# Optimization experiments

Hardware: AMD Instinct MI355X
Metric: run time of the kernel (lower is better)

## Reference

```python
import jax, jax.numpy as jnp
import numpy as np

N = 100000   # nodes
E = 1600000  # edges (avg degree 16)
D = 128      # in_feats == h_feats (residual requires equality)
RES = 0.2    # residual coefficient
EPS = 1e-5   # LayerNorm eps (torch default)
PROP_STEP = 3


def setup_inputs() -> dict:
    key = jax.random.key(0)
    ks = jax.random.split(key, 8)
    s = 1.0 / np.sqrt(D)
    return {
        "src": jax.random.randint(ks[0], (E,), 0, N),
        "dst": jax.random.randint(ks[1], (E,), 0, N),
        "in_feat": jax.random.normal(ks[2], (N, D), jnp.float32),
        # conv1 / conv2 GraphConv weights (Glorot-ish scale) and biases
        "W1": jax.random.normal(ks[3], (D, D), jnp.float32) * s,
        "b1": jnp.zeros((D,), jnp.float32),
        "W2": jax.random.normal(ks[4], (D, D), jnp.float32) * s,
        "b2": jnp.zeros((D,), jnp.float32),
        # LayerNorms used at loop steps i=1 and i=2 (norms[0] is unused by forward)
        "ln1_g": jnp.ones((D,), jnp.float32),
        "ln1_b": jnp.zeros((D,), jnp.float32),
        "ln2_g": jnp.ones((D,), jnp.float32),
        "ln2_b": jnp.zeros((D,), jnp.float32),
    }


def _gcn_conv(src, dst, x, W, b):
    # DGL GraphConv with norm='both': out = D_in^{-1/2} A D_out^{-1/2} X W + b
    ones_e = jnp.ones(src.shape[0], x.dtype)
    deg_out = jnp.maximum(jax.ops.segment_sum(ones_e, src, num_segments=N), 1.0)
    deg_in = jnp.maximum(jax.ops.segment_sum(ones_e, dst, num_segments=N), 1.0)
    xw = (x * jax.lax.rsqrt(deg_out)[:, None]) @ W           # [N, D]
    agg = jax.ops.segment_sum(xw[src], dst, num_segments=N)  # gather -> scatter-add
    return agg * jax.lax.rsqrt(deg_in)[:, None] + b


def _layer_norm(x, g, b):
    mu = jnp.mean(x, axis=-1, keepdims=True)
    var = jnp.mean(jnp.square(x - mu), axis=-1, keepdims=True)
    return (x - mu) * jax.lax.rsqrt(var + EPS) * g + b


def reference(src, dst, in_feat, W1, b1, W2, b2, ln1_g, ln1_b, ln2_g, ln2_b):
    h = _gcn_conv(src, dst, in_feat, W1, b1) + RES * in_feat
    for g_, b_ in ((ln1_g, ln1_b), (ln2_g, ln2_b)):  # steps i = 1 .. prop_step-1
        h = _layer_norm(h, g_, b_)
        h = jax.nn.relu(h)
        h = _gcn_conv(src, dst, h, W2, b2) + RES * in_feat
    return h
```

## Files before the change

kernel.cpp:

```cpp
#include <hip/hip_runtime.h>

#define NN 100000
#define DD 128
#define RESC 0.2f
#define EPSL 1e-5f
#define BSH 10
#define NBKT ((NN + 1023) >> BSH)

typedef _Float16 f16;
typedef _Float16 f16x2 __attribute__((ext_vector_type(2)));
typedef _Float16 f16x4 __attribute__((ext_vector_type(4)));
typedef _Float16 f16x8 __attribute__((ext_vector_type(8)));
typedef float f32x16 __attribute__((ext_vector_type(16)));

static __device__ __forceinline__ int swz(int r, int c_half) {
  return r * 256 + ((c_half * 2) ^ ((r & 15) << 4));
}

__global__ __launch_bounds__(256) void k_hist(const int* __restrict__ src,
                                              const int* __restrict__ dst,
                                              int* __restrict__ dego,
                                              int* __restrict__ bsum, int E) {
  __shared__ int cnt[NBKT];
  const int t = threadIdx.x;
  if (t < NBKT) cnt[t] = 0;
  __syncthreads();
  const int base = blockIdx.x * 4096 + t * 16;
#pragma unroll
  for (int q = 0; q < 4; ++q) {
    int idx = base + q * 4;
    int sv[4], dv[4];
    if (idx + 3 < E) {
      *(int4*)sv = *(const int4*)(src + idx);
      *(int4*)dv = *(const int4*)(dst + idx);
#pragma unroll
      for (int k = 0; k < 4; ++k) {
        atomicAdd(&dego[sv[k]], 1);
        atomicAdd(&cnt[dv[k] >> BSH], 1);
      }
    } else {
      for (int k = 0; k < 4 && idx + k < E; ++k) {
        atomicAdd(&dego[src[idx + k]], 1);
        atomicAdd(&cnt[dst[idx + k] >> BSH], 1);
      }
    }
  }
  __syncthreads();
  if (t < NBKT && cnt[t]) atomicAdd(&bsum[t], cnt[t]);
}

__global__ __launch_bounds__(128) void k_scan2(const int* __restrict__ bsum,
                                               int* __restrict__ bpre,
                                               int* __restrict__ bcur) {
  __shared__ int sh[128];
  const int t = threadIdx.x;
  int v = (t < NBKT) ? bsum[t] : 0;
  sh[t] = v;
  __syncthreads();
  for (int off = 1; off < 128; off <<= 1) {
    int add = (t >= off) ? sh[t - off] : 0;
    __syncthreads();
    sh[t] += add;
    __syncthreads();
  }
  if (t < NBKT) {
    int e = (t == 0) ? 0 : sh[t - 1];
    bpre[t] = e;
    bcur[t] = e;
  }
}

__global__ __launch_bounds__(256) void k_prep(const int* __restrict__ dego,
                                              float* __restrict__ rsq_o) {
  int i = blockIdx.x * 256 + threadIdx.x;
  if (i < NN) rsq_o[i] = rsqrtf((float)max(dego[i], 1));
}

__global__ __launch_bounds__(256) void k_wprep(const float* __restrict__ W,
                                               f16* __restrict__ Wt) {
  int i = blockIdx.x * 256 + threadIdx.x;
  int n = i >> 7, k = i & 127;
  Wt[(size_t)n * 128 + k] = (f16)W[(size_t)k * 128 + n];
}

__global__ __launch_bounds__(256) void k_binA(const int* __restrict__ src,
                                              const int* __restrict__ dst,
                                              int* __restrict__ bcur,
                                              int2* __restrict__ gpairs, int E) {
  __shared__ int cnt[NBKT], cnt2[NBKT], gofs[NBKT];
  const int t = threadIdx.x;
  if (t < NBKT) { cnt[t] = 0; cnt2[t] = 0; }
  __syncthreads();
  const int base = blockIdx.x * 4096 + t * 16;
  int sv[16], dv[16];
#pragma unroll
  for (int q = 0; q < 4; ++q) {
    int idx = base + q * 4;
    if (idx + 3 < E) {
      *(int4*)(sv + q * 4) = *(const int4*)(src + idx);
      *(int4*)(dv + q * 4) = *(const int4*)(dst + idx);
    } else {
#pragma unroll
      for (int k = 0; k < 4; ++k) {
        sv[q * 4 + k] = (idx + k < E) ? src[idx + k] : 0;
        dv[q * 4 + k] = (idx + k < E) ? dst[idx + k] : -1;
      }
    }
  }
#pragma unroll
  for (int j = 0; j < 16; ++j)
    if (base + j < E) atomicAdd(&cnt[dv[j] >> BSH], 1);
  __syncthreads();
  if (t < NBKT && cnt[t]) gofs[t] = atomicAdd(&bcur[t], cnt[t]);
  __syncthreads();
#pragma unroll
  for (int j = 0; j < 16; ++j)
    if (base + j < E) {
      int b = dv[j] >> BSH;
      int p = gofs[b] + atomicAdd(&cnt2[b], 1);
      gpairs[p] = make_int2(sv[j], dv[j]);
    }
}

__global__ __launch_bounds__(256) void k_binB(const int2* __restrict__ gpairs,
                                              const int* __restrict__ bpre,
                                              const int* __restrict__ bsum,
                                              int* __restrict__ rowp,
                                              float* __restrict__ rsq_i,
                                              int* __restrict__ colx, int E) {
  __shared__ int hist[1024];
  __shared__ int part[256];
  const int b = blockIdx.x, t = threadIdx.x;
  const int node0 = b << BSH;
  const int ebase = bpre[b], ecnt = bsum[b];
  for (int j = t; j < 1024; j += 256) hist[j] = 0;
  __syncthreads();
  for (int i = t; i < ecnt; i += 256)
    atomicAdd(&hist[gpairs[ebase + i].y - node0], 1);
  __syncthreads();
  const int j0 = t * 4;
  const int h0 = hist[j0], h1 = hist[j0 + 1], h2 = hist[j0 + 2], h3 = hist[j0 + 3];
  part[t] = h0 + h1 + h2 + h3;
  __syncthreads();
  for (int off = 1; off < 256; off <<= 1) {
    int add = (t >= off) ? part[t - off] : 0;
    __syncthreads();
    part[t] += add;
    __syncthreads();
  }
  int run = ebase + ((t == 0) ? 0 : part[t - 1]);
  const int pos[4] = {run, run + h0, run + h0 + h1, run + h0 + h1 + h2};
  const int hh[4] = {h0, h1, h2, h3};
#pragma unroll
  for (int k = 0; k < 4; ++k) {
    int node = node0 + j0 + k;
    if (node < NN) {
      rowp[node] = pos[k];
      rsq_i[node] = rsqrtf((float)max(hh[k], 1));
    }
  }
#pragma unroll
  for (int k = 0; k < 4; ++k) hist[j0 + k] = pos[k];
  __syncthreads();
  for (int i = t; i < ecnt; i += 256) {
    int2 pr = gpairs[ebase + i];
    int p = atomicAdd(&hist[pr.y - node0], 1);
    colx[p] = pr.x;
  }
  if (b == NBKT - 1 && t == 0) rowp[NN] = ebase + ecnt;
}

template <bool SCALE>
__global__ __launch_bounds__(256, 2) void k_gemm16(const void* __restrict__ inp,
                                                   const f16* __restrict__ Wt,
                                                   const float* __restrict__ rsq_o,
                                                   f16* __restrict__ out) {
  extern __shared__ char smem[];
  char* sX = smem;
  char* sW = smem + 32768;
  const int tid = threadIdx.x;
  const int row0 = blockIdx.x * 128;

#pragma unroll
  for (int i = 0; i < 8; ++i) {
    int chunk = i * 256 + tid;
    int r = chunk >> 4, cc = (chunk & 15) * 8;
    f16x8 v = *(const f16x8*)(Wt + (size_t)r * 128 + cc);
    *(f16x8*)(sW + swz(r, cc)) = v;
  }
#pragma unroll
  for (int i = 0; i < 8; ++i) {
    int chunk = i * 256 + tid;
    int r = chunk >> 4, cc = (chunk & 15) * 8;
    int grow = row0 + r;
    f16x8 v;
    if (SCALE) {
      const float* in = (const float*)inp;
      float4 v0 = {0, 0, 0, 0}, v1 = {0, 0, 0, 0};
      float s = 0.f;
      if (grow < NN) {
        v0 = *(const float4*)(in + (size_t)grow * DD + cc);
        v1 = *(const float4*)(in + (size_t)grow * DD + cc + 4);
        s = rsq_o[grow];
      }
      v[0] = (f16)(v0.x * s); v[1] = (f16)(v0.y * s);
      v[2] = (f16)(v0.z * s); v[3] = (f16)(v0.w * s);
      v[4] = (f16)(v1.x * s); v[5] = (f16)(v1.y * s);
      v[6] = (f16)(v1.z * s); v[7] = (f16)(v1.w * s);
    } else {
      const f16* in = (const f16*)inp;
      if (grow < NN) v = *(const f16x8*)(in + (size_t)grow * DD + cc);
      else { f16x8 z = {}; v = z; }
    }
    *(f16x8*)(sX + swz(r, cc)) = v;
  }
  __syncthreads();

  const int wv = tid >> 6, lane = tid & 63;
  const int am = lane & 31;
  const int kg = lane >> 5;
  f32x16 acc[4];
#pragma unroll
  for (int ct = 0; ct < 4; ++ct)
#pragma unroll
    for (int q = 0; q < 16; ++q) acc[ct][q] = 0.f;

  const int ar = wv * 32 + am;
#pragma unroll
  for (int ks = 0; ks < 8; ++ks) {
    const int kc = ks * 16 + kg * 8;
    f16x8 af = *(const f16x8*)(sX + swz(ar, kc));
#pragma unroll
    for (int ct = 0; ct < 4; ++ct) {
      f16x8 bf = *(const f16x8*)(sW + swz(ct * 32 + am, kc));
      acc[ct] = __builtin_amdgcn_mfma_f32_32x32x16_f16(af, bf, acc[ct], 0, 0, 0);
    }
  }

#pragma unroll
  for (int ct = 0; ct < 4; ++ct) {
#pragma unroll
    for (int reg = 0; reg < 16; ++reg) {
      int trow = (reg & 3) + 8 * (reg >> 2) + 4 * kg;
      int grow = row0 + wv * 32 + trow;
      if (grow < NN) out[(size_t)grow * DD + ct * 32 + am] = (f16)acc[ct][reg];
    }
  }
}

template <bool PRE>
__global__ __launch_bounds__(256) void k_gather(const f16* __restrict__ xw,
                                                const int* __restrict__ colx,
                                                const int* __restrict__ rowp,
                                                const float* __restrict__ rsq_i,
                                                const float* __restrict__ bias,
                                                const float* __restrict__ resid,
                                                const float* __restrict__ rsq_o,
                                                const float* __restrict__ g,
                                                const float* __restrict__ bb,
                                                void* __restrict__ outp) {
  const int wave = (blockIdx.x * 256 + threadIdx.x) >> 6;
  const int lane = threadIdx.x & 63;
  const int half = lane >> 5;
  const int l32 = lane & 31;
  if (wave >= NN) return;
  const int beg = rowp[wave], end = rowp[wave + 1];
  float4 a0 = {0, 0, 0, 0}, a1 = {0, 0, 0, 0}, a2 = {0, 0, 0, 0}, a3 = {0, 0, 0, 0};
  int e = beg + half;
  for (; e + 6 < end; e += 8) {
    int c0 = colx[e], c1 = colx[e + 2], c2 = colx[e + 4], c3 = colx[e + 6];
    f16x4 v0 = *(const f16x4*)(xw + (size_t)c0 * DD + l32 * 4);
    f16x4 v1 = *(const f16x4*)(xw + (size_t)c1 * DD + l32 * 4);
    f16x4 v2 = *(const f16x4*)(xw + (size_t)c2 * DD + l32 * 4);
    f16x4 v3 = *(const f16x4*)(xw + (size_t)c3 * DD + l32 * 4);
    a0.x += (float)v0[0]; a0.y += (float)v0[1]; a0.z += (float)v0[2]; a0.w += (float)v0[3];
    a1.x += (float)v1[0]; a1.y += (float)v1[1]; a1.z += (float)v1[2]; a1.w += (float)v1[3];
    a2.x += (float)v2[0]; a2.y += (float)v2[1]; a2.z += (float)v2[2]; a2.w += (float)v2[3];
    a3.x += (float)v3[0]; a3.y += (float)v3[1]; a3.z += (float)v3[2]; a3.w += (float)v3[3];
  }
  for (; e < end; e += 2) {
    int c = colx[e];
    f16x4 v = *(const f16x4*)(xw + (size_t)c * DD + l32 * 4);
    a0.x += (float)v[0]; a0.y += (float)v[1]; a0.z += (float)v[2]; a0.w += (float)v[3];
  }
  a0.x += a1.x + a2.x + a3.x;
  a0.y += a1.y + a2.y + a3.y;
  a0.z += a1.z + a2.z + a3.z;
  a0.w += a1.w + a2.w + a3.w;
  a0.x += __shfl_xor(a0.x, 32);
  a0.y += __shfl_xor(a0.y, 32);
  a0.z += __shfl_xor(a0.z, 32);
  a0.w += __shfl_xor(a0.w, 32);

  const float r = rsq_i[wave];
  float4 bv = *(const float4*)(bias + l32 * 4);
  float4 rf = *(const float4*)(resid + (size_t)wave * DD + l32 * 4);
  float4 o;
  o.x = a0.x * r + bv.x + RESC * rf.x;
  o.y = a0.y * r + bv.y + RESC * rf.y;
  o.z = a0.z * r + bv.z + RESC * rf.z;
  o.w = a0.w * r + bv.w + RESC * rf.w;

  if (PRE) {
    float s = o.x + o.y + o.z + o.w;
    float q = o.x * o.x + o.y * o.y + o.z * o.z + o.w * o.w;
#pragma unroll
    for (int off = 1; off < 32; off <<= 1) {
      s += __shfl_xor(s, off);
      q += __shfl_xor(q, off);
    }
    float mu = s * (1.f / 128.f);
    float var = q * (1.f / 128.f) - mu * mu;
    float rs = rsqrtf(var + EPSL);
    float sc = rsq_o[wave];
    float4 gv = *(const float4*)(g + l32 * 4);
    float4 lv = *(const float4*)(bb + l32 * 4);
    o.x = fmaxf((o.x - mu) * rs * gv.x + lv.x, 0.f) * sc;
    o.y = fmaxf((o.y - mu) * rs * gv.y + lv.y, 0.f) * sc;
    o.z = fmaxf((o.z - mu) * rs * gv.z + lv.z, 0.f) * sc;
    o.w = fmaxf((o.w - mu) * rs * gv.w + lv.w, 0.f) * sc;
    if (half == 0) {
      f16x4 o4;
      o4[0] = (f16)o.x; o4[1] = (f16)o.y; o4[2] = (f16)o.z; o4[3] = (f16)o.w;
      *(f16x4*)((f16*)outp + (size_t)wave * DD + l32 * 4) = o4;
    }
  } else {
    if (half == 0) *(float4*)((float*)outp + (size_t)wave * DD + l32 * 4) = o;
  }
}

extern "C" void kernel_launch(void* const* d_in, const int* in_sizes, int n_in,
                              void* d_out, int out_size, void* d_ws, size_t ws_size,
                              hipStream_t stream) {
  const int* src = (const int*)d_in[0];
  const int* dst = (const int*)d_in[1];
  const float* in_feat = (const float*)d_in[2];
  const float* W1 = (const float*)d_in[3];
  const float* b1 = (const float*)d_in[4];
  const float* W2 = (const float*)d_in[5];
  const float* b2 = (const float*)d_in[6];
  const float* g1 = (const float*)d_in[7];
  const float* lb1 = (const float*)d_in[8];
  const float* g2 = (const float*)d_in[9];
  const float* lb2 = (const float*)d_in[10];
  const int E = in_sizes[0];

  char* p = (char*)d_ws;
  auto alloc = [&](size_t bytes) {
    char* q = p;
    p += (bytes + 255) & ~(size_t)255;
    return q;
  };
  f16*   xw    = (f16*)alloc((size_t)NN * DD * 2);
  f16*   hb    = (f16*)alloc((size_t)NN * DD * 2);
  float* rsq_o = (float*)alloc((size_t)NN * 4);
  float* rsq_i = (float*)alloc((size_t)NN * 4);
  int*   dego  = (int*)alloc((size_t)NN * 4);
  int*   rowp  = (int*)alloc((size_t)(NN + 1) * 4);
  int*   colx  = (int*)alloc((size_t)E * 4);
  int*   bsum  = (int*)alloc((size_t)NBKT * 4);
  int*   bpre  = (int*)alloc((size_t)NBKT * 4);
  int*   bcur  = (int*)alloc((size_t)NBKT * 4);
  f16*   Wt1   = (f16*)alloc((size_t)DD * DD * 2);
  f16*   Wt2   = (f16*)alloc((size_t)DD * DD * 2);
  if ((size_t)(p - (char*)d_ws) > ws_size) return;
  int2* gpairs = (int2*)xw;

  hipMemsetAsync(dego, 0, (size_t)NN * 4, stream);
  hipMemsetAsync(bsum, 0, (size_t)NBKT * 4, stream);

  const int eb = (E + 4095) / 4096;
  k_hist<<<eb, 256, 0, stream>>>(src, dst, dego, bsum, E);
  k_scan2<<<1, 128, 0, stream>>>(bsum, bpre, bcur);
  k_prep<<<(NN + 255) / 256, 256, 0, stream>>>(dego, rsq_o);
  k_wprep<<<64, 256, 0, stream>>>(W1, Wt1);
  k_wprep<<<64, 256, 0, stream>>>(W2, Wt2);
  k_binA<<<eb, 256, 0, stream>>>(src, dst, bcur, gpairs, E);
  k_binB<<<NBKT, 256, 0, stream>>>(gpairs, bpre, bsum, rowp, rsq_i, colx, E);

  const int gblk = (NN + 127) / 128;
  const int agblk = (NN * 64 + 255) / 256;
  const size_t ldsb = 65536;

  k_gemm16<true><<<gblk, 256, ldsb, stream>>>(in_feat, Wt1, rsq_o, xw);
  k_gather<true><<<agblk, 256, 0, stream>>>(xw, colx, rowp, rsq_i, b1, in_feat, rsq_o, g1, lb1, hb);
  k_gemm16<false><<<gblk, 256, ldsb, stream>>>(hb, Wt2, rsq_o, xw);
  k_gather<true><<<agblk, 256, 0, stream>>>(xw, colx, rowp, rsq_i, b2, in_feat, rsq_o, g2, lb2, hb);
  k_gemm16<false><<<gblk, 256, ldsb, stream>>>(hb, Wt2, rsq_o, xw);
  k_gather<false><<<agblk, 256, 0, stream>>>(xw, colx, rowp, rsq_i, b2, in_feat, rsq_o, nullptr, nullptr, d_out);
}
```

Before: 520.8 us.

## Fuse gather+LayerNorm into GEMM and replace bucket scan with fixed slabs

The preprocessing drops the separate histogram, scan and prep kernels. Each destination bucket now gets a fixed slab of SLAB edges, so offsets no longer need a prefix sum, and out-degree counting is folded into the binning pass. The per-layer gather, LayerNorm and ReLU are fused with the following GEMM: each block aggregates its 128 rows into shared memory and then runs MFMA, which removes the intermediate hb round trip and a launch. The cost is a fixed per-bucket capacity that silently drops edges if a bucket overflows, and a gather phase with only 8 waves per CU of parallelism inside the GEMM kernel.

Measured after the change: 756.1 us. 45.2% more time.

```diff
diff --git a/kernel.cpp b/kernel.cpp
--- a/kernel.cpp
+++ b/kernel.cpp
@@ -6,87 +6,32 @@
 #define EPSL 1e-5f
 #define BSH 10
 #define NBKT ((NN + 1023) >> BSH)
+#define SLAB 20480
 
 typedef _Float16 f16;
-typedef _Float16 f16x2 __attribute__((ext_vector_type(2)));
 typedef _Float16 f16x4 __attribute__((ext_vector_type(4)));
 typedef _Float16 f16x8 __attribute__((ext_vector_type(8)));
 typedef float f32x16 __attribute__((ext_vector_type(16)));
 
-static __device__ __forceinline__ int swz(int r, int c_half) {
-  return r * 256 + ((c_half * 2) ^ ((r & 15) << 4));
-}
-
-__global__ __launch_bounds__(256) void k_hist(const int* __restrict__ src,
-                                              const int* __restrict__ dst,
-                                              int* __restrict__ dego,
-                                              int* __restrict__ bsum, int E) {
-  __shared__ int cnt[NBKT];
-  const int t = threadIdx.x;
-  if (t < NBKT) cnt[t] = 0;
-  __syncthreads();
-  const int base = blockIdx.x * 4096 + t * 16;
-#pragma unroll
-  for (int q = 0; q < 4; ++q) {
-    int idx = base + q * 4;
-    int sv[4], dv[4];
-    if (idx + 3 < E) {
-      *(int4*)sv = *(const int4*)(src + idx);
-      *(int4*)dv = *(const int4*)(dst + idx);
-#pragma unroll
-      for (int k = 0; k < 4; ++k) {
-        atomicAdd(&dego[sv[k]], 1);
-        atomicAdd(&cnt[dv[k] >> BSH], 1);
-      }
-    } else {
-      for (int k = 0; k < 4 && idx + k < E; ++k) {
-        atomicAdd(&dego[src[idx + k]], 1);
-        atomicAdd(&cnt[dst[idx + k] >> BSH], 1);
-      }
-    }
-  }
-  __syncthreads();
-  if (t < NBKT && cnt[t]) atomicAdd(&bsum[t], cnt[t]);
-}
-
-__global__ __launch_bounds__(128) void k_scan2(const int* __restrict__ bsum,
-                                               int* __restrict__ bpre,
+static __device__ __forceinline__ int swzb(int r, int b) {
+  return r * 256 + (b ^ ((r & 15) << 4));
+}
+
+__global__ __launch_bounds__(256) void k_wprep(const float* __restrict__ W1, const float* __restrict__ W2,
+                                               f16* __restrict__ Wt1, f16* __restrict__ Wt2,
                                                int* __restrict__ bcur) {
-  __shared__ int sh[128];
-  const int t = threadIdx.x;
-  int v = (t < NBKT) ? bsum[t] : 0;
-  sh[t] = v;
-  __syncthreads();
-  for (int off = 1; off < 128; off <<= 1) {
-    int add = (t >= off) ? sh[t - off] : 0;
-    __syncthreads();
-    sh[t] += add;
-    __syncthreads();
-  }
-  if (t < NBKT) {
-    int e = (t == 0) ? 0 : sh[t - 1];
-    bpre[t] = e;
-    bcur[t] = e;
-  }
-}
-
-__global__ __launch_bounds__(256) void k_prep(const int* __restrict__ dego,
-                                              float* __restrict__ rsq_o) {
   int i = blockIdx.x * 256 + threadIdx.x;
-  if (i < NN) rsq_o[i] = rsqrtf((float)max(dego[i], 1));
-}
-
-__global__ __launch_bounds__(256) void k_wprep(const float* __restrict__ W,
-                                               f16* __restrict__ Wt) {
-  int i = blockIdx.x * 256 + threadIdx.x;
-  int n = i >> 7, k = i & 127;
-  Wt[(size_t)n * 128 + k] = (f16)W[(size_t)k * 128 + n];
-}
-
-__global__ __launch_bounds__(256) void k_binA(const int* __restrict__ src,
-                                              const int* __restrict__ dst,
-                                              int* __restrict__ bcur,
-                                              int2* __restrict__ gpairs, int E) {
+  if (i < NBKT) bcur[i] = i * SLAB;
+  int w = i >> 14, j = i & 16383;
+  int n = j >> 7, k = j & 127;
+  const float* W = w ? W2 : W1;
+  f16* Wt = w ? Wt2 : Wt1;
+  Wt[n * 128 + k] = (f16)W[k * 128 + n];
+}
+
+__global__ __launch_bounds__(256) void k_histA(const int* __restrict__ src, const int* __restrict__ dst,
+                                               int* __restrict__ dego, int* __restrict__ bcur,
+                                               int2* __restrict__ gpairs, int E) {
   __shared__ int cnt[NBKT], cnt2[NBKT], gofs[NBKT];
   const int t = threadIdx.x;
   if (t < NBKT) { cnt[t] = 0; cnt2[t] = 0; }
@@ -109,7 +54,10 @@
   }
 #pragma unroll
   for (int j = 0; j < 16; ++j)
-    if (base + j < E) atomicAdd(&cnt[dv[j] >> BSH], 1);
+    if (base + j < E) {
+      atomicAdd(&dego[sv[j]], 1);
+      atomicAdd(&cnt[dv[j] >> BSH], 1);
+    }
   __syncthreads();
   if (t < NBKT && cnt[t]) gofs[t] = atomicAdd(&bcur[t], cnt[t]);
   __syncthreads();
@@ -118,21 +66,21 @@
     if (base + j < E) {
       int b = dv[j] >> BSH;
       int p = gofs[b] + atomicAdd(&cnt2[b], 1);
-      gpairs[p] = make_int2(sv[j], dv[j]);
-    }
-}
-
-__global__ __launch_bounds__(256) void k_binB(const int2* __restrict__ gpairs,
-                                              const int* __restrict__ bpre,
-                                              const int* __restrict__ bsum,
-                                              int* __restrict__ rowp,
-                                              float* __restrict__ rsq_i,
-                                              int* __restrict__ colx, int E) {
+      if (p < (b + 1) * SLAB) gpairs[p] = make_int2(sv[j], dv[j]);
+    }
+}
+
+__global__ __launch_bounds__(256) void k_binB(const int2* __restrict__ gpairs, const int* __restrict__ bcur,
+                                              const int* __restrict__ dego,
+                                              int* __restrict__ rowp, int* __restrict__ rend,
+                                              float* __restrict__ rsq_i, float* __restrict__ rsq_o,
+                                              int* __restrict__ colx) {
   __shared__ int hist[1024];
   __shared__ int part[256];
   const int b = blockIdx.x, t = threadIdx.x;
   const int node0 = b << BSH;
-  const int ebase = bpre[b], ecnt = bsum[b];
+  const int ebase = b * SLAB;
+  const int ecnt = min(bcur[b] - ebase, SLAB);
   for (int j = t; j < 1024; j += 256) hist[j] = 0;
   __syncthreads();
   for (int i = t; i < ecnt; i += 256)
@@ -156,7 +104,9 @@
     int node = node0 + j0 + k;
     if (node < NN) {
       rowp[node] = pos[k];
+      rend[node] = pos[k] + hh[k];
       rsq_i[node] = rsqrtf((float)max(hh[k], 1));
+      rsq_o[node] = rsqrtf((float)max(dego[node], 1));
     }
   }
 #pragma unroll
@@ -167,104 +117,173 @@
     int p = atomicAdd(&hist[pr.y - node0], 1);
     colx[p] = pr.x;
   }
-  if (b == NBKT - 1 && t == 0) rowp[NN] = ebase + ecnt;
-}
-
-template <bool SCALE>
-__global__ __launch_bounds__(256, 2) void k_gemm16(const void* __restrict__ inp,
-                                                   const f16* __restrict__ Wt,
-                                                   const float* __restrict__ rsq_o,
-                                                   f16* __restrict__ out) {
+}
+
+static __device__ __forceinline__ void mfma_store(const char* sX, const char* sW, f16* __restrict__ out,
+                                                  int row0, int tid) {
+  const int wv = tid >> 6, lane = tid & 63;
+  const int am = lane & 31;
+  const int kg = lane >> 5;
+  f32x16 acc[4];
+#pragma unroll
+  for (int ct = 0; ct < 4; ++ct)
+#pragma unroll
+    for (int q = 0; q < 16; ++q) acc[ct][q] = 0.f;
+
+  const int ar = wv * 32 + am;
+#pragma unroll
+  for (int ks = 0; ks < 8; ++ks) {
+    const int kc = ks * 16 + kg * 8;
+    f16x8 af = *(const f16x8*)(sX + swzb(ar, kc * 2));
+#pragma unroll
+    for (int ct = 0; ct < 4; ++ct) {
+      f16x8 bf = *(const f16x8*)(sW + swzb(ct * 32 + am, kc * 2));
+      acc[ct] = __builtin_amdgcn_mfma_f32_32x32x16_f16(af, bf, acc[ct], 0, 0, 0);
+    }
+  }
+#pragma unroll
+  for (int ct = 0; ct < 4; ++ct) {
+#pragma unroll
+    for (int reg = 0; reg < 16; ++reg) {
+      int trow = (reg & 3) + 8 * (reg >> 2) + 4 * kg;
+      int grow = row0 + wv * 32 + trow;
+      if (grow < NN) out[(size_t)grow * DD + ct * 32 + am] = (f16)acc[ct][reg];
+    }
+  }
+}
+
+__global__ __launch_bounds__(256, 2) void k_gemm1(const float* __restrict__ in, const f16* __restrict__ Wt,
+                                                  const float* __restrict__ rsq_o, f16* __restrict__ out) {
   extern __shared__ char smem[];
   char* sX = smem;
   char* sW = smem + 32768;
   const int tid = threadIdx.x;
   const int row0 = blockIdx.x * 128;
-
 #pragma unroll
   for (int i = 0; i < 8; ++i) {
     int chunk = i * 256 + tid;
     int r = chunk >> 4, cc = (chunk & 15) * 8;
-    f16x8 v = *(const f16x8*)(Wt + (size_t)r * 128 + cc);
-    *(f16x8*)(sW + swz(r, cc)) = v;
+    *(f16x8*)(sW + swzb(r, cc * 2)) = *(const f16x8*)(Wt + (size_t)r * 128 + cc);
   }
 #pragma unroll
   for (int i = 0; i < 8; ++i) {
     int chunk = i * 256 + tid;
     int r = chunk >> 4, cc = (chunk & 15) * 8;
     int grow = row0 + r;
+    float4 v0 = {0, 0, 0, 0}, v1 = {0, 0, 0, 0};
+    float s = 0.f;
+    if (grow < NN) {
+      v0 = *(const float4*)(in + (size_t)grow * DD + cc);
+      v1 = *(const float4*)(in + (size_t)grow * DD + cc + 4);
+      s = rsq_o[grow];
+    }
     f16x8 v;
-    if (SCALE) {
-      const float* in = (const float*)inp;
-      float4 v0 = {0, 0, 0, 0}, v1 = {0, 0, 0, 0};
-      float s = 0.f;
-      if (grow < NN) {
-        v0 = *(const float4*)(in + (size_t)grow * DD + cc);
-        v1 = *(const float4*)(in + (size_t)grow * DD + cc + 4);
-        s = rsq_o[grow];
+    v[0] = (f16)(v0.x * s); v[1] = (f16)(v0.y * s);
+    v[2] = (f16)(v0.z * s); v[3] = (f16)(v0.w * s);
+    v[4] = (f16)(v1.x * s); v[5] = (f16)(v1.y * s);
+    v[6] = (f16)(v1.z * s); v[7] = (f16)(v1.w * s);
+    *(f16x8*)(sX + swzb(r, cc * 2)) = v;
+  }
+  __syncthreads();
+  mfma_store(sX, sW, out, row0, tid);
+}
+
+__global__ __launch_bounds__(256, 2) void k_conv(const f16* __restrict__ xw, const int* __restrict__ colx,
+                                                 const int* __restrict__ rowp, const int* __restrict__ rend,
+                                                 const float* __restrict__ rsq_i, const float* __restrict__ bias,
+                                                 const float* __restrict__ resid, const float* __restrict__ rsq_o,
+                                                 const float* __restrict__ g, const float* __restrict__ bb,
+                                                 const f16* __restrict__ Wt, f16* __restrict__ out) {
+  extern __shared__ char smem[];
+  char* sX = smem;
+  char* sW = smem + 32768;
+  const int tid = threadIdx.x;
+  const int row0 = blockIdx.x * 128;
+#pragma unroll
+  for (int i = 0; i < 8; ++i) {
+    int chunk = i * 256 + tid;
+    int r = chunk >> 4, cc = (chunk & 15) * 8;
+    *(f16x8*)(sW + swzb(r, cc * 2)) = *(const f16x8*)(Wt + (size_t)r * 128 + cc);
+  }
+  const int wv = tid >> 6, lane = tid & 63;
+  const int half = lane >> 5, l32 = lane & 31;
+  const float4 bv = *(const float4*)(bias + l32 * 4);
+  const float4 gv = *(const float4*)(g + l32 * 4);
+  const float4 lv = *(const float4*)(bb + l32 * 4);
+
+  for (int i = 0; i < 32; ++i) {
+    const int node = row0 + wv * 32 + i;
+    const int r = wv * 32 + i;
+    f16x4 o4 = {};
+    if (node < NN) {
+      const int beg = rowp[node], end = rend[node];
+      float4 a0 = {0, 0, 0, 0}, a1 = {0, 0, 0, 0}, a2 = {0, 0, 0, 0}, a3 = {0, 0, 0, 0};
+      int e = beg + half;
+      for (; e + 6 < end; e += 8) {
+        int c0 = colx[e], c1 = colx[e + 2], c2 = colx[e + 4], c3 = colx[e + 6];
+        f16x4 v0 = *(const f16x4*)(xw + (size_t)c0 * DD + l32 * 4);
+        f16x4 v1 = *(const f16x4*)(xw + (size_t)c1 * DD + l32 * 4);
+        f16x4 v2 = *(const f16x4*)(xw + (size_t)c2 * DD + l32 * 4);
+        f16x4 v3 = *(const f16x4*)(xw + (size_t)c3 * DD + l32 * 4);
+        a0.x += (float)v0[0]; a0.y += (float)v0[1]; a0.z += (float)v0[2]; a0.w += (float)v0[3];
+        a1.x += (float)v1[0]; a1.y += (float)v1[1]; a1.z += (float)v1[2]; a1.w += (float)v1[3];
+        a2.x += (float)v2[0]; a2.y += (float)v2[1]; a2.z += (float)v2[2]; a2.w += (float)v2[3];
+        a3.x += (float)v3[0]; a3.y += (float)v3[1]; a3.z += (float)v3[2]; a3.w += (float)v3[3];
       }
-      v[0] = (f16)(v0.x * s); v[1] = (f16)(v0.y * s);
-      v[2] = (f16)(v0.z * s); v[3] = (f16)(v0.w * s);
-      v[4] = (f16)(v1.x * s); v[5] = (f16)(v1.y * s);
-      v[6] = (f16)(v1.z * s); v[7] = (f16)(v1.w * s);
-    } else {
-      const f16* in = (const f16*)inp;
-      if (grow < NN) v = *(const f16x8*)(in + (size_t)grow * DD + cc);
-      else { f16x8 z = {}; v = z; }
-    }
-    *(f16x8*)(sX + swz(r, cc)) = v;
-  }
-  __syncthreads();
-
-  const int wv = tid >> 6, lane = tid & 63;
-  const int am = lane & 31;
-  const int kg = lane >> 5;
-  f32x16 acc[4];
-#pragma unroll
-  for (int ct = 0; ct < 4; ++ct)
-#pragma unroll
-    for (int q = 0; q < 16; ++q) acc[ct][q] = 0.f;
-
-  const int ar = wv * 32 + am;
-#pragma unroll
-  for (int ks = 0; ks < 8; ++ks) {
-    const int kc = ks * 16 + kg * 8;
-    f16x8 af = *(const f16x8*)(sX + swz(ar, kc));
-#pragma unroll
-    for (int ct = 0; ct < 4; ++ct) {
-      f16x8 bf = *(const f16x8*)(sW + swz(ct * 32 + am, kc));
-      acc[ct] = __builtin_amdgcn_mfma_f32_32x32x16_f16(af, bf, acc[ct], 0, 0, 0);
-    }
-  }
-
-#pragma unroll
-  for (int ct = 0; ct < 4; ++ct) {
-#pragma unroll
-    for (int reg = 0; reg < 16; ++reg) {
-      int trow = (reg & 3) + 8 * (reg >> 2) + 4 * kg;
-      int grow = row0 + wv * 32 + trow;
-      if (grow < NN) out[(size_t)grow * DD + ct * 32 + am] = (f16)acc[ct][reg];
-    }
-  }
-}
-
-template <bool PRE>
-__global__ __launch_bounds__(256) void k_gather(const f16* __restrict__ xw,
-                                                const int* __restrict__ colx,
-                                                const int* __restrict__ rowp,
-                                                const float* __restrict__ rsq_i,
-                                                const float* __restrict__ bias,
-                                                const float* __restrict__ resid,
-                                                const float* __restrict__ rsq_o,
-                                                const float* __restrict__ g,
-                                                const float* __restrict__ bb,
-                                                void* __restrict__ outp) {
+      for (; e < end; e += 2) {
+        int c = colx[e];
+        f16x4 v = *(const f16x4*)(xw + (size_t)c * DD + l32 * 4);
+        a0.x += (float)v[0]; a0.y += (float)v[1]; a0.z += (float)v[2]; a0.w += (float)v[3];
+      }
+      a0.x += a1.x + a2.x + a3.x;
+      a0.y += a1.y + a2.y + a3.y;
+      a0.z += a1.z + a2.z + a3.z;
+      a0.w += a1.w + a2.w + a3.w;
+      a0.x += __shfl_xor(a0.x, 32);
+      a0.y += __shfl_xor(a0.y, 32);
+      a0.z += __shfl_xor(a0.z, 32);
+      a0.w += __shfl_xor(a0.w, 32);
+
+      const float rI = rsq_i[node];
+      const float4 rf = *(const float4*)(resid + (size_t)node * DD + l32 * 4);
+      float4 o;
+      o.x = a0.x * rI + bv.x + RESC * rf.x;
+      o.y = a0.y * rI + bv.y + RESC * rf.y;
+      o.z = a0.z * rI + bv.z + RESC * rf.z;
+      o.w = a0.w * rI + bv.w + RESC * rf.w;
+
+      float s = o.x + o.y + o.z + o.w;
+      float q = o.x * o.x + o.y * o.y + o.z * o.z + o.w * o.w;
+#pragma unroll
+      for (int off = 1; off < 32; off <<= 1) {
+        s += __shfl_xor(s, off);
+        q += __shfl_xor(q, off);
+      }
+      float mu = s * (1.f / 128.f);
+      float var = q * (1.f / 128.f) - mu * mu;
+      float rs = rsqrtf(var + EPSL);
+      float sc = rsq_o[node];
+      o4[0] = (f16)(fmaxf((o.x - mu) * rs * gv.x + lv.x, 0.f) * sc);
+      o4[1] = (f16)(fmaxf((o.y - mu) * rs * gv.y + lv.y, 0.f) * sc);
+      o4[2] = (f16)(fmaxf((o.z - mu) * rs * gv.z + lv.z, 0.f) * sc);
+      o4[3] = (f16)(fmaxf((o.w - mu) * rs * gv.w + lv.w, 0.f) * sc);
+    }
+    if (half == 0) *(f16x4*)(sX + swzb(r, l32 * 8)) = o4;
+  }
+  __syncthreads();
+  mfma_store(sX, sW, out, row0, tid);
+}
+
+__global__ __launch_bounds__(256) void k_gatherF(const f16* __restrict__ xw, const int* __restrict__ colx,
+                                                 const int* __restrict__ rowp, const int* __restrict__ rend,
+                                                 const float* __restrict__ rsq_i, const float* __restrict__ bias,
+                                                 const float* __restrict__ resid, float* __restrict__ out) {
   const int wave = (blockIdx.x * 256 + threadIdx.x) >> 6;
   const int lane = threadIdx.x & 63;
   const int half = lane >> 5;
   const int l32 = lane & 31;
   if (wave >= NN) return;
-  const int beg = rowp[wave], end = rowp[wave + 1];
+  const int beg = rowp[wave], end = rend[wave];
   float4 a0 = {0, 0, 0, 0}, a1 = {0, 0, 0, 0}, a2 = {0, 0, 0, 0}, a3 = {0, 0, 0, 0};
   int e = beg + half;
   for (; e + 6 < end; e += 8) {
@@ -291,41 +310,16 @@
   a0.y += __shfl_xor(a0.y, 32);
   a0.z += __shfl_xor(a0.z, 32);
   a0.w += __shfl_xor(a0.w, 32);
-
-  const float r = rsq_i[wave];
-  float4 bv = *(const float4*)(bias + l32 * 4);
-  float4 rf = *(const float4*)(resid + (size_t)wave * DD + l32 * 4);
-  float4 o;
-  o.x = a0.x * r + bv.x + RESC * rf.x;
-  o.y = a0.y * r + bv.y + RESC * rf.y;
-  o.z = a0.z * r + bv.z + RESC * rf.z;
-  o.w = a0.w * r + bv.w + RESC * rf.w;
-
-  if (PRE) {
-    float s = o.x + o.y + o.z + o.w;
-    float q = o.x * o.x + o.y * o.y + o.z * o.z + o.w * o.w;
-#pragma unroll
-    for (int off = 1; off < 32; off <<= 1) {
-      s += __shfl_xor(s, off);
-      q += __shfl_xor(q, off);
-    }
-    float mu = s * (1.f / 128.f);
-    float var = q * (1.f / 128.f) - mu * mu;
-    float rs = rsqrtf(var + EPSL);
-    float sc = rsq_o[wave];
-    float4 gv = *(const float4*)(g + l32 * 4);
-    float4 lv = *(const float4*)(bb + l32 * 4);
-    o.x = fmaxf((o.x - mu) * rs * gv.x + lv.x, 0.f) * sc;
-    o.y = fmaxf((o.y - mu) * rs * gv.y + lv.y, 0.f) * sc;
-    o.z = fmaxf((o.z - mu) * rs * gv.z + lv.z, 0.f) * sc;
-    o.w = fmaxf((o.w - mu) * rs * gv.w + lv.w, 0.f) * sc;
-    if (half == 0) {
-      f16x4 o4;
-      o4[0] = (f16)o.x; o4[1] = (f16)o.y; o4[2] = (f16)o.z; o4[3] = (f16)o.w;
-      *(f16x4*)((f16*)outp + (size_t)wave * DD + l32 * 4) = o4;
-    }
-  } else {
-    if (half == 0) *(float4*)((float*)outp + (size_t)wave * DD + l32 * 4) = o;
+  if (half == 0) {
+    const float r = rsq_i[wave];
+    float4 bv = *(const float4*)(bias + l32 * 4);
+    float4 rf = *(const float4*)(resid + (size_t)wave * DD + l32 * 4);
+    float4 o;
+    o.x = a0.x * r + bv.x + RESC * rf.x;
+    o.y = a0.y * r + bv.y + RESC * rf.y;
+    o.z = a0.z * r + bv.z + RESC * rf.z;
+    o.w = a0.w * r + bv.w + RESC * rf.w;
+    *(float4*)(out + (size_t)wave * DD + l32 * 4) = o;
   }
 }
 
@@ -351,41 +345,33 @@
     p += (bytes + 255) & ~(size_t)255;
     return q;
   };
-  f16*   xw    = (f16*)alloc((size_t)NN * DD * 2);
-  f16*   hb    = (f16*)alloc((size_t)NN * DD * 2);
+  f16*   xw_a  = (f16*)alloc((size_t)NN * DD * 2);
+  f16*   xw_b  = (f16*)alloc((size_t)NN * DD * 2);
+  int*   colx  = (int*)alloc((size_t)NBKT * SLAB * 4);
+  int*   rowp  = (int*)alloc((size_t)NN * 4);
+  int*   rend  = (int*)alloc((size_t)NN * 4);
+  float* rsq_i = (float*)alloc((size_t)NN * 4);
   float* rsq_o = (float*)alloc((size_t)NN * 4);
-  float* rsq_i = (float*)alloc((size_t)NN * 4);
   int*   dego  = (int*)alloc((size_t)NN * 4);
-  int*   rowp  = (int*)alloc((size_t)(NN + 1) * 4);
-  int*   colx  = (int*)alloc((size_t)E * 4);
-  int*   bsum  = (int*)alloc((size_t)NBKT * 4);
-  int*   bpre  = (int*)alloc((size_t)NBKT * 4);
   int*   bcur  = (int*)alloc((size_t)NBKT * 4);
   f16*   Wt1   = (f16*)alloc((size_t)DD * DD * 2);
   f16*   Wt2   = (f16*)alloc((size_t)DD * DD * 2);
   if ((size_t)(p - (char*)d_ws) > ws_size) return;
-  int2* gpairs = (int2*)xw;
+  int2* gpairs = (int2*)xw_a;
 
   hipMemsetAsync(dego, 0, (size_t)NN * 4, stream);
-  hipMemsetAsync(bsum, 0, (size_t)NBKT * 4, stream);
 
   const int eb = (E + 4095) / 4096;
-  k_hist<<<eb, 256, 0, stream>>>(src, dst, dego, bsum, E);
-  k_scan2<<<1, 128, 0, stream>>>(bsum, bpre, bcur);
-  k_prep<<<(NN + 255) / 256, 256, 0, stream>>>(dego, rsq_o);
-  k_wprep<<<64, 256, 0, stream>>>(W1, Wt1);
-  k_wprep<<<64, 256, 0, stream>>>(W2, Wt2);
-  k_binA<<<eb, 256, 0, stream>>>(src, dst, bcur, gpairs, E);
-  k_binB<<<NBKT, 256, 0, stream>>>(gpairs, bpre, bsum, rowp, rsq_i, colx, E);
+  k_wprep<<<128, 256, 0, stream>>>(W1, W2, Wt1, Wt2, bcur);
+  k_histA<<<eb, 256, 0, stream>>>(src, dst, dego, bcur, gpairs, E);
+  k_binB<<<NBKT, 256, 0, stream>>>(gpairs, bcur, dego, rowp, rend, rsq_i, rsq_o, colx);
 
   const int gblk = (NN + 127) / 128;
   const int agblk = (NN * 64 + 255) / 256;
   const size_t ldsb = 65536;
 
-  k_gemm16<true><<<gblk, 256, ldsb, stream>>>(in_feat, Wt1, rsq_o, xw);
-  k_gather<true><<<agblk, 256, 0, stream>>>(xw, colx, rowp, rsq_i, b1, in_feat, rsq_o, g1, lb1, hb);
-  k_gemm16<false><<<gblk, 256, ldsb, stream>>>(hb, Wt2, rsq_o, xw);
-  k_gather<true><<<agblk, 256, 0, stream>>>(xw, colx, rowp, rsq_i, b2, in_feat, rsq_o, g2, lb2, hb);
-  k_gemm16<false><<<gblk, 256, ldsb, stream>>>(hb, Wt2, rsq_o, xw);
-  k_gather<false><<<agblk, 256, 0, stream>>>(xw, colx, rowp, rsq_i, b2, in_feat, rsq_o, nullptr, nullptr, d_out);
-}
+  k_gemm1<<<gblk, 256, ldsb, stream>>>(in_feat, Wt1, rsq_o, xw_a);
+  k_conv<<<gblk, 256, ldsb, stream>>>(xw_a, colx, rowp, rend, rsq_i, b1, in_feat, rsq_o, g1, lb1, Wt2, xw_b);
+  k_conv<<<gblk, 256, ldsb, stream>>>(xw_b, colx, rowp, rend, rsq_i, b2, in_feat, rsq_o, g2, lb2, Wt2, xw_a);
+  k_gatherF<<<agblk, 256, 0, stream>>>(xw_a, colx, rowp, rend, rsq_i, b2, in_feat, (float*)d_out);
+}
```
